# Performance work log

Measured on AMD Instinct MI355X. Metric: run time of the kernel, lower is better.

## Reference

```python
import jax, jax.numpy as jnp
import numpy as np

D_MODEL = 1024
D_INTERNAL = 64
SEQ = 2048
BATCH = 4


def setup_inputs() -> dict:
    key = jax.random.key(0)
    ks = jax.random.split(key, 9)
    s = 1.0 / np.sqrt(D_MODEL)
    return {
        "query": jax.random.normal(ks[0], (SEQ, BATCH, D_MODEL), jnp.float32),
        "key": jax.random.normal(ks[1], (SEQ, BATCH, D_MODEL), jnp.float32),
        "value": jax.random.normal(ks[2], (SEQ, BATCH, D_MODEL), jnp.float32),
        "Wq": jax.random.normal(ks[3], (D_MODEL, D_INTERNAL), jnp.float32) * s,
        "bq": jnp.zeros((D_INTERNAL,), jnp.float32),
        "Wk": jax.random.normal(ks[4], (D_MODEL, D_INTERNAL), jnp.float32) * s,
        "bk": jnp.zeros((D_INTERNAL,), jnp.float32),
        "Wv": jax.random.normal(ks[5], (D_MODEL, D_MODEL), jnp.float32) * s,
        "bv": jnp.zeros((D_MODEL,), jnp.float32),
    }


def reference(query, key, value, Wq, bq, Wk, bk, Wv, bv):
    # inputs: (S, B, D); project then move batch first -> (B, S, *)
    q = (query @ Wq + bq).transpose(1, 0, 2)          # (B, S, d_int)
    k = (key @ Wk + bk).transpose(1, 0, 2)            # (B, S, d_int)
    v = (value @ Wv + bv).transpose(1, 0, 2)          # (B, S, D)
    scores = jnp.einsum("bqd,bkd->bqk", q, k) / jnp.sqrt(jnp.float32(D_INTERNAL))
    probs = jax.nn.softmax(scores, axis=-1)           # row softmax over keys
    # extra renormalization over the QUERY axis (dim=1), as in the source
    probs = probs / (1e-9 + probs.sum(axis=1, keepdims=True))
    aten = jnp.einsum("bqk,bkd->bqd", probs, v).transpose(1, 0, 2)  # (S, B, D)
    return aten, probs
```

## Files before the change

### kernel.cpp

```cpp
#include <hip/hip_runtime.h>
#include <math.h>

#define SEQ 2048
#define BATCH 4
#define DM 1024
#define DI 64

typedef __attribute__((ext_vector_type(8))) short bf16x8;
typedef __attribute__((ext_vector_type(4))) float f32x4;

__device__ __forceinline__ unsigned short f2bf(float f) {
  unsigned u = __float_as_uint(f);
  unsigned r = (u + 0x7fff + ((u >> 16) & 1)) >> 16;
  return (unsigned short)r;
}

__device__ __forceinline__ float bf2f(unsigned short u) {
  return __uint_as_float((unsigned)u << 16);
}

__device__ __forceinline__ void gload_lds16(const void* g, void* l) {
  __builtin_amdgcn_global_load_lds(
      (const __attribute__((address_space(1))) unsigned int*)g,
      (__attribute__((address_space(3))) unsigned int*)l, 16, 0, 0);
}


__global__ __launch_bounds__(256) void trans_kernel(
    const float* __restrict__ Wq, const float* __restrict__ Wk,
    const float* __restrict__ Wv,
    unsigned short* __restrict__ WqkT, unsigned short* __restrict__ WvT) {
  __shared__ unsigned short t[64][65];
  int lx = threadIdx.x & 63, ly = threadIdx.x >> 6;
  if (blockIdx.y < 16) {
    int bx = blockIdx.x * 64, by = blockIdx.y * 64;
#pragma unroll
    for (int i = 0; i < 64; i += 4)
      t[ly + i][lx] = f2bf(Wv[(size_t)(bx + ly + i) * DM + by + lx]);
    __syncthreads();
#pragma unroll
    for (int i = 0; i < 64; i += 4)
      WvT[(size_t)(by + ly + i) * DM + bx + lx] = t[lx][ly + i];
  } else {
    int which = blockIdx.y - 16;
    const float* W = which ? Wk : Wq;
    unsigned short* WT = WqkT + (size_t)which * DI * DM;
    int bx = blockIdx.x * 64;
#pragma unroll
    for (int i = 0; i < 64; i += 4)
      t[ly + i][lx] = f2bf(W[(size_t)(bx + ly + i) * DI + lx]);
    __syncthreads();
#pragma unroll
    for (int i = 0; i < 64; i += 4)
      WT[(size_t)(ly + i) * DM + bx + lx] = t[lx][ly + i];
  }
}

__global__ __launch_bounds__(256) void qkproj_mfma(
    const float* __restrict__ query, const float* __restrict__ key,
    const unsigned short* __restrict__ WqkT,
    const float* __restrict__ bq, const float* __restrict__ bk,
    unsigned short* __restrict__ qbf, unsigned short* __restrict__ kbf) {
  __shared__ __align__(16) unsigned short As[32 * 32];
  __shared__ __align__(16) unsigned short Bs[64 * 32];
  int which = blockIdx.y;
  const float* A = (which ? key : query) + (size_t)blockIdx.x * 32 * DM;
  const unsigned short* Bt = WqkT + (size_t)which * DI * DM;
  const float* bias = which ? bk : bq;
  unsigned short* outp = which ? kbf : qbf;

  const int tid = threadIdx.x;
  const int lane = tid & 63, wave = tid >> 6;
  const int lrow = lane & 15, quad = lane >> 4;
  const int wr = (wave >> 1) * 16;
  const int wc = (wave & 1) * 32;
  const int sw = (quad ^ ((lrow >> 1) & 3)) * 8;
  f32x4 acc[2] = {};

  const int am = tid >> 3, asub = tid & 7;
  const int akc = asub * 4;
  const int asl = am * 32 + (((asub >> 1) ^ ((am >> 1) & 3)) * 8) + (asub & 1) * 4;
  const int bn = tid >> 2;
  const int bkc = (((tid & 3) ^ ((bn >> 1) & 3)) * 8);

  for (int k0 = 0; k0 < DM; k0 += 32) {
    __syncthreads();
    gload_lds16(Bt + (size_t)bn * DM + k0 + bkc, Bs + wave * 512);
    float4 a = *(const float4*)(A + (size_t)am * DM + k0 + akc);
    ushort4 h;
    h.x = f2bf(a.x); h.y = f2bf(a.y); h.z = f2bf(a.z); h.w = f2bf(a.w);
    *(ushort4*)&As[asl] = h;
    __syncthreads();
    bf16x8 af = *(const bf16x8*)&As[(wr + lrow) * 32 + sw];
    bf16x8 b0 = *(const bf16x8*)&Bs[(wc + lrow) * 32 + sw];
    bf16x8 b1 = *(const bf16x8*)&Bs[(wc + 16 + lrow) * 32 + sw];
    acc[0] = __builtin_amdgcn_mfma_f32_16x16x32_bf16(af, b0, acc[0], 0, 0, 0);
    acc[1] = __builtin_amdgcn_mfma_f32_16x16x32_bf16(af, b1, acc[1], 0, 0, 0);
  }
  int sbase = blockIdx.x * 8 + (wr >> 2) + quad;
#pragma unroll
  for (int ni = 0; ni < 2; ++ni) {
    int n = wc + ni * 16 + lrow;
    float bb = bias[n];
#pragma unroll
    for (int reg = 0; reg < 4; ++reg)
      outp[((size_t)reg * SEQ + sbase) * DI + n] = f2bf(acc[ni][reg] + bb);
  }
}

__global__ __launch_bounds__(256) void vcast_kernel(
    const float* __restrict__ value, unsigned short* __restrict__ vbf) {
  size_t i = ((size_t)blockIdx.x * 256 + threadIdx.x) * 8;
  float4 a = *(const float4*)(value + i);
  float4 b = *(const float4*)(value + i + 4);
  bf16x8 h;
  h[0] = (short)f2bf(a.x); h[1] = (short)f2bf(a.y);
  h[2] = (short)f2bf(a.z); h[3] = (short)f2bf(a.w);
  h[4] = (short)f2bf(b.x); h[5] = (short)f2bf(b.y);
  h[6] = (short)f2bf(b.z); h[7] = (short)f2bf(b.w);
  *(bf16x8*)(vbf + i) = h;
}

__device__ __forceinline__ void mfma_core_bb_12864(
    const unsigned short* __restrict__ At, int lda,
    const unsigned short* __restrict__ Bt, int ldb,
    int K, f32x4 (&acc)[4][2],
    unsigned short* As, unsigned short* Bs) {
  const int tid  = threadIdx.x;
  const int lane = tid & 63;
  const int wave = tid >> 6;
  const int wr   = (wave >> 1) * 64;
  const int wc   = (wave & 1) * 32;
  const int lrow = lane & 15;
  const int quad = lane >> 4;
  const int sw   = (quad ^ ((lrow >> 1) & 3)) * 8;
  const int bn   = tid >> 2;
  const int bkc  = ((tid & 3) ^ ((bn >> 1) & 3)) * 8;

  for (int k0 = 0; k0 < K; k0 += 32) {
    __syncthreads();
#pragma unroll
    for (int it = 0; it < 2; ++it) {
      int c = it * 256 + tid;
      int m = c >> 2, kc = ((c & 3) ^ ((m >> 1) & 3)) * 8;
      gload_lds16(At + (size_t)m * lda + k0 + kc,
                  As + (size_t)(it * 256 + wave * 64) * 8);
    }
    gload_lds16(Bt + (size_t)bn * ldb + k0 + bkc, Bs + wave * 512);
    __syncthreads();
    bf16x8 af[4], bfr[2];
#pragma unroll
    for (int mi = 0; mi < 4; ++mi)
      af[mi] = *(const bf16x8*)&As[(wr + mi * 16 + lrow) * 32 + sw];
#pragma unroll
    for (int ni = 0; ni < 2; ++ni)
      bfr[ni] = *(const bf16x8*)&Bs[(wc + ni * 16 + lrow) * 32 + sw];
#pragma unroll
    for (int mi = 0; mi < 4; ++mi)
#pragma unroll
      for (int ni = 0; ni < 2; ++ni)
        acc[mi][ni] = __builtin_amdgcn_mfma_f32_16x16x32_bf16(
            af[mi], bfr[ni], acc[mi][ni], 0, 0, 0);
  }
}

__global__ __launch_bounds__(256) void vproj_mfma(
    const unsigned short* __restrict__ vbf, const unsigned short* __restrict__ WvT,
    const float* __restrict__ bv, unsigned short* __restrict__ vT) {
  __shared__ __align__(16) unsigned short As[128 * 32];
  __shared__ __align__(16) unsigned short Bs[64 * 32];
  __shared__ __align__(16) unsigned short ep[64 * 4 * 32];
  f32x4 acc[4][2] = {};
  int m0 = blockIdx.x * 128, n0 = blockIdx.y * 64;
  mfma_core_bb_12864(vbf + (size_t)m0 * DM, DM, WvT + (size_t)n0 * DM, DM, DM,
                     acc, As, Bs);
  const int tid = threadIdx.x;
  const int lane = tid & 63, wave = tid >> 6;
  const int wr = (wave >> 1) * 64, wc = (wave & 1) * 32;
  const int lrow = lane & 15, quad = lane >> 4;
#pragma unroll
  for (int mi = 0; mi < 4; ++mi) {
    int ss = (wr >> 2) + mi * 4 + quad;
#pragma unroll
    for (int ni = 0; ni < 2; ++ni) {
      int nn = wc + ni * 16 + lrow;
      float bias = bv[n0 + nn];
      int swz = (nn & 3) << 3;
#pragma unroll
      for (int reg = 0; reg < 4; ++reg)
        ep[nn * 128 + reg * 32 + (ss ^ swz)] = f2bf(acc[mi][ni][reg] + bias);
    }
  }
  __syncthreads();
  int s0 = m0 >> 2;
#pragma unroll
  for (int t8 = 0; t8 < 4; ++t8) {
    int c = t8 * 256 + tid;
    int ss8 = (c & 3) * 8, b = (c >> 2) & 3, nn = c >> 4;
    uint4 vv = *(const uint4*)&ep[nn * 128 + b * 32 + (ss8 ^ ((nn & 3) << 3))];
    *(uint4*)&vT[((size_t)(b * DM + n0 + nn)) * SEQ + s0 + ss8] = vv;
  }
}

__global__ __launch_bounds__(256) void scores_rowpanel(
    const unsigned short* __restrict__ qbf, const unsigned short* __restrict__ kbf,
    unsigned short* __restrict__ ebf, float* __restrict__ invrs) {
  __shared__ __align__(16) unsigned short Qs[16 * 64];
  __shared__ __align__(16) unsigned short Ks[128 * 64];
  __shared__ float red[4][16];
  int bid = blockIdx.x;
  int x = bid & 7, j = bid >> 3;
  int b = x >> 1;
  int q0 = (j * 2 + (x & 1)) * 16;

  const int tid = threadIdx.x;
  const int lane = tid & 63, wave = tid >> 6;
  const int lrow = lane & 15, quad = lane >> 4;
  const int wc = wave * 32;
  const int sw = (quad ^ ((lrow >> 1) & 3)) * 8;
  const unsigned short* Q = qbf + ((size_t)b * SEQ + q0) * DI;
  const unsigned short* Kp = kbf + (size_t)b * SEQ * DI;
  unsigned short* C = ebf + (size_t)b * SEQ * SEQ;

  if (tid < 128) {
    int m = tid >> 3, kk = (tid >> 2) & 1, jj = tid & 3;
    gload_lds16(Q + (size_t)m * DI + kk * 32 + ((jj ^ ((m >> 1) & 3)) * 8),
                Qs + (size_t)(tid & ~63) * 8);
  }

  float rsum[4] = {0.f, 0.f, 0.f, 0.f};
  for (int kt = 0; kt < 16; ++kt) {
    int k0 = kt * 128;
    __syncthreads();
#pragma unroll
    for (int it = 0; it < 4; ++it) {
      int c = it * 256 + tid;
      int n = c >> 3, kk = (c >> 2) & 1, jj = c & 3;
      gload_lds16(Kp + (size_t)(k0 + n) * DI + kk * 32 + ((jj ^ ((n >> 1) & 3)) * 8),
                  Ks + (size_t)(it * 256 + wave * 64) * 8);
    }
    __syncthreads();
    bf16x8 af[2], bfr[2][2];
#pragma unroll
    for (int kk = 0; kk < 2; ++kk) {
      af[kk] = *(const bf16x8*)&Qs[lrow * 64 + kk * 32 + sw];
#pragma unroll
      for (int ni = 0; ni < 2; ++ni)
        bfr[ni][kk] = *(const bf16x8*)&Ks[(wc + ni * 16 + lrow) * 64 + kk * 32 + sw];
    }
    f32x4 acc[2] = {};
#pragma unroll
    for (int ni = 0; ni < 2; ++ni) {
      acc[ni] = __builtin_amdgcn_mfma_f32_16x16x32_bf16(af[0], bfr[ni][0], acc[ni], 0, 0, 0);
      acc[ni] = __builtin_amdgcn_mfma_f32_16x16x32_bf16(af[1], bfr[ni][1], acc[ni], 0, 0, 0);
    }
#pragma unroll
    for (int ni = 0; ni < 2; ++ni) {
      int n = k0 + wc + ni * 16 + lrow;
#pragma unroll
      for (int reg = 0; reg < 4; ++reg) {
        float e = __expf(acc[ni][reg] * 0.125f);
        C[(size_t)(q0 + quad * 4 + reg) * SEQ + n] = f2bf(e);
        rsum[reg] += e;
      }
    }
  }
#pragma unroll
  for (int reg = 0; reg < 4; ++reg) {
    rsum[reg] += __shfl_xor(rsum[reg], 1);
    rsum[reg] += __shfl_xor(rsum[reg], 2);
    rsum[reg] += __shfl_xor(rsum[reg], 4);
    rsum[reg] += __shfl_xor(rsum[reg], 8);
  }
  if (lrow == 0) {
#pragma unroll
    for (int reg = 0; reg < 4; ++reg) red[wave][quad * 4 + reg] = rsum[reg];
  }
  __syncthreads();
  if (tid < 16) {
    float t = red[0][tid] + red[1][tid] + red[2][tid] + red[3][tid];
    invrs[(size_t)b * SEQ + q0 + tid] = 1.0f / t;
  }
}

__global__ void zero_kernel(float* __restrict__ p, int n) {
  int i = blockIdx.x * blockDim.x + threadIdx.x;
  if (i < n) p[i] = 0.f;
}

__global__ void recip_kernel(const float* __restrict__ in,
                             float* __restrict__ outp, float eps, int n) {
  int i = blockIdx.x * blockDim.x + threadIdx.x;
  if (i < n) outp[i] = 1.0f / (eps + in[i]);
}

__global__ __launch_bounds__(256) void colsum_kernel(
    const unsigned short* __restrict__ ebf, const float* __restrict__ invrs,
    float* __restrict__ colsum) {
  int b = blockIdx.z;
  int k = blockIdx.x * 256 + threadIdx.x;
  int q0 = blockIdx.y * 128;
  const unsigned short* p = ebf + (size_t)b * SEQ * SEQ + (size_t)q0 * SEQ + k;
  const float* ir = invrs + (size_t)b * SEQ + q0;
  float sum = 0.f;
#pragma unroll 4
  for (int i = 0; i < 128; ++i) sum += bf2f(p[(size_t)i * SEQ]) * ir[i];
  atomicAdd(&colsum[b * SEQ + k], sum);
}

__global__ __launch_bounds__(256) void vscale_kernel(
    unsigned short* __restrict__ vT, const float* __restrict__ invcol) {
  size_t i = ((size_t)blockIdx.x * 256 + threadIdx.x) * 8;
  int s = (int)(i & (SEQ - 1));
  int b = (int)(i >> 21);
  bf16x8 v = *(const bf16x8*)(vT + i);
  const float* ic = invcol + (size_t)b * SEQ + s;
  float4 c0 = *(const float4*)(ic);
  float4 c1 = *(const float4*)(ic + 4);
  bf16x8 r;
  r[0] = (short)f2bf(bf2f((unsigned short)v[0]) * c0.x);
  r[1] = (short)f2bf(bf2f((unsigned short)v[1]) * c0.y);
  r[2] = (short)f2bf(bf2f((unsigned short)v[2]) * c0.z);
  r[3] = (short)f2bf(bf2f((unsigned short)v[3]) * c0.w);
  r[4] = (short)f2bf(bf2f((unsigned short)v[4]) * c1.x);
  r[5] = (short)f2bf(bf2f((unsigned short)v[5]) * c1.y);
  r[6] = (short)f2bf(bf2f((unsigned short)v[6]) * c1.z);
  r[7] = (short)f2bf(bf2f((unsigned short)v[7]) * c1.w);
  *(bf16x8*)(vT + i) = r;
}

__global__ __launch_bounds__(256) void probsout_kernel(
    const unsigned short* __restrict__ ebf, const float* __restrict__ invrs,
    const float* __restrict__ invcol, float* __restrict__ probs) {
  size_t f = ((size_t)blockIdx.x * 256 + threadIdx.x) * 4;
  int b = (int)(f >> 22);
  int q = (int)((f >> 11) & 2047);
  int k = (int)(f & 2047);
  ushort4 h = *(const ushort4*)(ebf + f);
  float ir = invrs[b * SEQ + q];
  float4 c = *(const float4*)(invcol + b * SEQ + k);
  float4 p;
  p.x = bf2f(h.x) * ir * c.x;
  p.y = bf2f(h.y) * ir * c.y;
  p.z = bf2f(h.z) * ir * c.z;
  p.w = bf2f(h.w) * ir * c.w;
  *(float4*)(probs + f) = p;
}

__global__ __launch_bounds__(256) void aten_mfma(
    const unsigned short* __restrict__ ebf, const unsigned short* __restrict__ vT,
    const float* __restrict__ invrs, float* __restrict__ out) {
  __shared__ __align__(16) unsigned short As[128 * 64];
  __shared__ __align__(16) unsigned short Bs[128 * 64];
  __shared__ float irs[128];
  int bid = blockIdx.x;
  int wg = (bid & 7) * 64 + (bid >> 3);
  int mb = wg & 15, nb = (wg >> 4) & 7, b = wg >> 7;
  int m0 = mb * 128, n0 = nb * 128;
  if (threadIdx.x < 128)
    irs[threadIdx.x] = invrs[(size_t)b * SEQ + m0 + threadIdx.x];
  const unsigned short* At = ebf + ((size_t)b * SEQ + m0) * SEQ;
  const unsigned short* Bt = vT + ((size_t)b * DM + n0) * SEQ;

  const int tid = threadIdx.x;
  const int lane = tid & 63, wave = tid >> 6;
  const int wr = (wave >> 1) * 64, wc = (wave & 1) * 64;
  const int lrow = lane & 15, quad = lane >> 4;
  const int sw = (quad ^ ((lrow >> 1) & 3)) * 8;

  f32x4 acc[4][4] = {};
  for (int k0 = 0; k0 < SEQ; k0 += 64) {
    __syncthreads();
#pragma unroll
    for (int it = 0; it < 4; ++it) {
      int c = it * 256 + tid;
      int m = c >> 3, kk = (c >> 2) & 1, jj = c & 3;
      gload_lds16(At + (size_t)m * SEQ + k0 + kk * 32 + ((jj ^ ((m >> 1) & 3)) * 8),
                  As + (size_t)(it * 256 + wave * 64) * 8);
    }
#pragma unroll
    for (int it = 0; it < 4; ++it) {
      int c = it * 256 + tid;
      int n = c >> 3, kk = (c >> 2) & 1, jj = c & 3;
      gload_lds16(Bt + (size_t)n * SEQ + k0 + kk * 32 + ((jj ^ ((n >> 1) & 3)) * 8),
                  Bs + (size_t)(it * 256 + wave * 64) * 8);
    }
    __syncthreads();
    bf16x8 bfr[4][2];
#pragma unroll
    for (int ni = 0; ni < 4; ++ni)
#pragma unroll
      for (int kk = 0; kk < 2; ++kk)
        bfr[ni][kk] = *(const bf16x8*)&Bs[(wc + ni * 16 + lrow) * 64 + kk * 32 + sw];
#pragma unroll
    for (int mi = 0; mi < 4; ++mi) {
      bf16x8 a0 = *(const bf16x8*)&As[(wr + mi * 16 + lrow) * 64 + sw];
      bf16x8 a1 = *(const bf16x8*)&As[(wr + mi * 16 + lrow) * 64 + 32 + sw];
#pragma unroll
      for (int ni = 0; ni < 4; ++ni) {
        acc[mi][ni] = __builtin_amdgcn_mfma_f32_16x16x32_bf16(a0, bfr[ni][0], acc[mi][ni], 0, 0, 0);
        acc[mi][ni] = __builtin_amdgcn_mfma_f32_16x16x32_bf16(a1, bfr[ni][1], acc[mi][ni], 0, 0, 0);
      }
    }
  }
#pragma unroll
  for (int mi = 0; mi < 4; ++mi) {
    int rb = wr + mi * 16 + quad * 4;
    int qr = m0 + rb;
#pragma unroll
    for (int ni = 0; ni < 4; ++ni) {
      int n = n0 + wc + ni * 16 + lrow;
#pragma unroll
      for (int reg = 0; reg < 4; ++reg)
        out[(size_t)(qr + reg) * (BATCH * DM) + b * DM + n] =
            acc[mi][ni][reg] * irs[rb + reg];
    }
  }
}

extern "C" void kernel_launch(void* const* d_in, const int* in_sizes, int n_in,
                              void* d_out, int out_size, void* d_ws, size_t ws_size,
                              hipStream_t stream) {
  const float* query = (const float*)d_in[0];
  const float* key   = (const float*)d_in[1];
  const float* value = (const float*)d_in[2];
  const float* Wq    = (const float*)d_in[3];
  const float* bq    = (const float*)d_in[4];
  const float* Wk    = (const float*)d_in[5];
  const float* bk    = (const float*)d_in[6];
  const float* Wv    = (const float*)d_in[7];
  const float* bv    = (const float*)d_in[8];

  float* out   = (float*)d_out;
  float* probs = out + (size_t)SEQ * BATCH * DM;

  unsigned short* WvT  = (unsigned short*)d_ws;
  unsigned short* WqkT = WvT  + (size_t)DM * DM;
  unsigned short* qbf  = WqkT + (size_t)2 * DI * DM;
  unsigned short* kbf  = qbf  + (size_t)BATCH * SEQ * DI;
  unsigned short* vT   = kbf  + (size_t)BATCH * SEQ * DI;
  unsigned short* ebf  = vT   + (size_t)BATCH * DM * SEQ;
  unsigned short* vbf  = ebf;
  float* colsum = (float*)(ebf + (size_t)BATCH * SEQ * SEQ);
  float* invrs  = colsum + (size_t)BATCH * SEQ;
  float* invcol = invrs  + (size_t)BATCH * SEQ;

  trans_kernel<<<dim3(16, 18), 256, 0, stream>>>(Wq, Wk, Wv, WqkT, WvT);
  qkproj_mfma<<<dim3(SEQ * BATCH / 32, 2), 256, 0, stream>>>(
      query, key, WqkT, bq, bk, qbf, kbf);
  vcast_kernel<<<(SEQ * BATCH * DM / 8) / 256, 256, 0, stream>>>(value, vbf);
  vproj_mfma<<<dim3(SEQ * BATCH / 128, DM / 64), 256, 0, stream>>>(vbf, WvT, bv, vT);
  scores_rowpanel<<<dim3(512), 256, 0, stream>>>(qbf, kbf, ebf, invrs);
  zero_kernel<<<(BATCH * SEQ + 255) / 256, 256, 0, stream>>>(colsum, BATCH * SEQ);
  colsum_kernel<<<dim3(SEQ / 256, SEQ / 128, BATCH), 256, 0, stream>>>(
      ebf, invrs, colsum);
  recip_kernel<<<(BATCH * SEQ + 255) / 256, 256, 0, stream>>>(
      colsum, invcol, 1e-9f, BATCH * SEQ);
  vscale_kernel<<<(BATCH * DM * SEQ / 8) / 256, 256, 0, stream>>>(vT, invcol);
  aten_mfma<<<dim3(512), 256, 0, stream>>>(ebf, vT, invrs, out);
  probsout_kernel<<<(BATCH * SEQ * SEQ / 4) / 256, 256, 0, stream>>>(
      ebf, invrs, invcol, probs);
}
```

Measured before the change: 327.3 us.

## Fuse column-sum into scores kernel and column scaling into V projection

The column-sum pass over the exp-score matrix is folded into the scores kernel, where each block re-reads its freshly written 16-row panel and atomically adds scaled column partials. The V-projection epilogue now multiplies by the inverse column sums, so the separate vscale pass over vT is removed. The colsum zeroing moves into the weight-transpose kernel. vbf gets its own workspace region so the V projection can run after the scores. This cuts three launches and two full passes over large buffers. In exchange there are more atomics (8 per thread per block), a re-read of the panel inside the scores kernel, and a larger workspace.

Result: slower. 334.2 us (+2.1%).

```diff
diff --git a/kernel.cpp b/kernel.cpp
--- a/kernel.cpp
+++ b/kernel.cpp
@@ -29,7 +29,8 @@
 __global__ __launch_bounds__(256) void trans_kernel(
     const float* __restrict__ Wq, const float* __restrict__ Wk,
     const float* __restrict__ Wv,
-    unsigned short* __restrict__ WqkT, unsigned short* __restrict__ WvT) {
+    unsigned short* __restrict__ WqkT, unsigned short* __restrict__ WvT,
+    float* __restrict__ colsum) {
   __shared__ unsigned short t[64][65];
   int lx = threadIdx.x & 63, ly = threadIdx.x >> 6;
   if (blockIdx.y < 16) {
@@ -41,7 +42,7 @@
 #pragma unroll
     for (int i = 0; i < 64; i += 4)
       WvT[(size_t)(by + ly + i) * DM + bx + lx] = t[lx][ly + i];
-  } else {
+  } else if (blockIdx.y < 18) {
     int which = blockIdx.y - 16;
     const float* W = which ? Wk : Wq;
     unsigned short* WT = WqkT + (size_t)which * DI * DM;
@@ -53,6 +54,10 @@
 #pragma unroll
     for (int i = 0; i < 64; i += 4)
       WT[(size_t)(ly + i) * DM + bx + lx] = t[lx][ly + i];
+  } else {
+    int idx = blockIdx.x * 256 + threadIdx.x;
+    colsum[idx] = 0.f;
+    colsum[idx + 4096] = 0.f;
   }
 }
 
@@ -166,12 +171,17 @@
 
 __global__ __launch_bounds__(256) void vproj_mfma(
     const unsigned short* __restrict__ vbf, const unsigned short* __restrict__ WvT,
-    const float* __restrict__ bv, unsigned short* __restrict__ vT) {
+    const float* __restrict__ bv, const float* __restrict__ invcol,
+    unsigned short* __restrict__ vT) {
   __shared__ __align__(16) unsigned short As[128 * 32];
   __shared__ __align__(16) unsigned short Bs[64 * 32];
   __shared__ __align__(16) unsigned short ep[64 * 4 * 32];
+  __shared__ float icl[128];
   f32x4 acc[4][2] = {};
   int m0 = blockIdx.x * 128, n0 = blockIdx.y * 64;
+  int s0 = m0 >> 2;
+  if (threadIdx.x < 128)
+    icl[threadIdx.x] = invcol[(size_t)(threadIdx.x >> 5) * SEQ + s0 + (threadIdx.x & 31)];
   mfma_core_bb_12864(vbf + (size_t)m0 * DM, DM, WvT + (size_t)n0 * DM, DM, DM,
                      acc, As, Bs);
   const int tid = threadIdx.x;
@@ -188,11 +198,11 @@
       int swz = (nn & 3) << 3;
 #pragma unroll
       for (int reg = 0; reg < 4; ++reg)
-        ep[nn * 128 + reg * 32 + (ss ^ swz)] = f2bf(acc[mi][ni][reg] + bias);
+        ep[nn * 128 + reg * 32 + (ss ^ swz)] =
+            f2bf((acc[mi][ni][reg] + bias) * icl[reg * 32 + ss]);
     }
   }
   __syncthreads();
-  int s0 = m0 >> 2;
 #pragma unroll
   for (int t8 = 0; t8 < 4; ++t8) {
     int c = t8 * 256 + tid;
@@ -204,10 +214,12 @@
 
 __global__ __launch_bounds__(256) void scores_rowpanel(
     const unsigned short* __restrict__ qbf, const unsigned short* __restrict__ kbf,
-    unsigned short* __restrict__ ebf, float* __restrict__ invrs) {
+    unsigned short* __restrict__ ebf, float* __restrict__ invrs,
+    float* __restrict__ colsum) {
   __shared__ __align__(16) unsigned short Qs[16 * 64];
   __shared__ __align__(16) unsigned short Ks[128 * 64];
   __shared__ float red[4][16];
+  __shared__ float irl[16];
   int bid = blockIdx.x;
   int x = bid & 7, j = bid >> 3;
   int b = x >> 1;
@@ -265,6 +277,7 @@
       }
     }
   }
+  __threadfence_block();
 #pragma unroll
   for (int reg = 0; reg < 4; ++reg) {
     rsum[reg] += __shfl_xor(rsum[reg], 1);
@@ -279,54 +292,33 @@
   __syncthreads();
   if (tid < 16) {
     float t = red[0][tid] + red[1][tid] + red[2][tid] + red[3][tid];
-    invrs[(size_t)b * SEQ + q0 + tid] = 1.0f / t;
-  }
-}
-
-__global__ void zero_kernel(float* __restrict__ p, int n) {
-  int i = blockIdx.x * blockDim.x + threadIdx.x;
-  if (i < n) p[i] = 0.f;
+    float inv = 1.0f / t;
+    invrs[(size_t)b * SEQ + q0 + tid] = inv;
+    irl[tid] = inv;
+  }
+  __syncthreads();
+  int k8 = tid * 8;
+  float cs[8] = {0.f, 0.f, 0.f, 0.f, 0.f, 0.f, 0.f, 0.f};
+#pragma unroll 4
+  for (int i = 0; i < 16; ++i) {
+    const unsigned short* row = C + (size_t)(q0 + i) * SEQ + k8;
+    ushort4 h0 = *(const ushort4*)(row);
+    ushort4 h1 = *(const ushort4*)(row + 4);
+    float ir = irl[i];
+    cs[0] += bf2f(h0.x) * ir; cs[1] += bf2f(h0.y) * ir;
+    cs[2] += bf2f(h0.z) * ir; cs[3] += bf2f(h0.w) * ir;
+    cs[4] += bf2f(h1.x) * ir; cs[5] += bf2f(h1.y) * ir;
+    cs[6] += bf2f(h1.z) * ir; cs[7] += bf2f(h1.w) * ir;
+  }
+#pragma unroll
+  for (int jj = 0; jj < 8; ++jj)
+    atomicAdd(&colsum[b * SEQ + k8 + jj], cs[jj]);
 }
 
 __global__ void recip_kernel(const float* __restrict__ in,
                              float* __restrict__ outp, float eps, int n) {
   int i = blockIdx.x * blockDim.x + threadIdx.x;
   if (i < n) outp[i] = 1.0f / (eps + in[i]);
-}
-
-__global__ __launch_bounds__(256) void colsum_kernel(
-    const unsigned short* __restrict__ ebf, const float* __restrict__ invrs,
-    float* __restrict__ colsum) {
-  int b = blockIdx.z;
-  int k = blockIdx.x * 256 + threadIdx.x;
-  int q0 = blockIdx.y * 128;
-  const unsigned short* p = ebf + (size_t)b * SEQ * SEQ + (size_t)q0 * SEQ + k;
-  const float* ir = invrs + (size_t)b * SEQ + q0;
-  float sum = 0.f;
-#pragma unroll 4
-  for (int i = 0; i < 128; ++i) sum += bf2f(p[(size_t)i * SEQ]) * ir[i];
-  atomicAdd(&colsum[b * SEQ + k], sum);
-}
-
-__global__ __launch_bounds__(256) void vscale_kernel(
-    unsigned short* __restrict__ vT, const float* __restrict__ invcol) {
-  size_t i = ((size_t)blockIdx.x * 256 + threadIdx.x) * 8;
-  int s = (int)(i & (SEQ - 1));
-  int b = (int)(i >> 21);
-  bf16x8 v = *(const bf16x8*)(vT + i);
-  const float* ic = invcol + (size_t)b * SEQ + s;
-  float4 c0 = *(const float4*)(ic);
-  float4 c1 = *(const float4*)(ic + 4);
-  bf16x8 r;
-  r[0] = (short)f2bf(bf2f((unsigned short)v[0]) * c0.x);
-  r[1] = (short)f2bf(bf2f((unsigned short)v[1]) * c0.y);
-  r[2] = (short)f2bf(bf2f((unsigned short)v[2]) * c0.z);
-  r[3] = (short)f2bf(bf2f((unsigned short)v[3]) * c0.w);
-  r[4] = (short)f2bf(bf2f((unsigned short)v[4]) * c1.x);
-  r[5] = (short)f2bf(bf2f((unsigned short)v[5]) * c1.y);
-  r[6] = (short)f2bf(bf2f((unsigned short)v[6]) * c1.z);
-  r[7] = (short)f2bf(bf2f((unsigned short)v[7]) * c1.w);
-  *(bf16x8*)(vT + i) = r;
 }
 
 __global__ __launch_bounds__(256) void probsout_kernel(
@@ -440,23 +432,20 @@
   unsigned short* kbf  = qbf  + (size_t)BATCH * SEQ * DI;
   unsigned short* vT   = kbf  + (size_t)BATCH * SEQ * DI;
   unsigned short* ebf  = vT   + (size_t)BATCH * DM * SEQ;
-  unsigned short* vbf  = ebf;
-  float* colsum = (float*)(ebf + (size_t)BATCH * SEQ * SEQ);
+  unsigned short* vbf  = ebf  + (size_t)BATCH * SEQ * SEQ;
+  float* colsum = (float*)(vbf + (size_t)BATCH * SEQ * DM);
   float* invrs  = colsum + (size_t)BATCH * SEQ;
   float* invcol = invrs  + (size_t)BATCH * SEQ;
 
-  trans_kernel<<<dim3(16, 18), 256, 0, stream>>>(Wq, Wk, Wv, WqkT, WvT);
+  trans_kernel<<<dim3(16, 19), 256, 0, stream>>>(Wq, Wk, Wv, WqkT, WvT, colsum);
   qkproj_mfma<<<dim3(SEQ * BATCH / 32, 2), 256, 0, stream>>>(
       query, key, WqkT, bq, bk, qbf, kbf);
   vcast_kernel<<<(SEQ * BATCH * DM / 8) / 256, 256, 0, stream>>>(value, vbf);
-  vproj_mfma<<<dim3(SEQ * BATCH / 128, DM / 64), 256, 0, stream>>>(vbf, WvT, bv, vT);
-  scores_rowpanel<<<dim3(512), 256, 0, stream>>>(qbf, kbf, ebf, invrs);
-  zero_kernel<<<(BATCH * SEQ + 255) / 256, 256, 0, stream>>>(colsum, BATCH * SEQ);
-  colsum_kernel<<<dim3(SEQ / 256, SEQ / 128, BATCH), 256, 0, stream>>>(
-      ebf, invrs, colsum);
+  scores_rowpanel<<<dim3(512), 256, 0, stream>>>(qbf, kbf, ebf, invrs, colsum);
   recip_kernel<<<(BATCH * SEQ + 255) / 256, 256, 0, stream>>>(
       colsum, invcol, 1e-9f, BATCH * SEQ);
-  vscale_kernel<<<(BATCH * DM * SEQ / 8) / 256, 256, 0, stream>>>(vT, invcol);
+  vproj_mfma<<<dim3(SEQ * BATCH / 128, DM / 64), 256, 0, stream>>>(
+      vbf, WvT, bv, invcol, vT);
   aten_mfma<<<dim3(512), 256, 0, stream>>>(ebf, vT, invrs, out);
   probsout_kernel<<<(BATCH * SEQ * SEQ / 4) / 256, 256, 0, stream>>>(
       ebf, invrs, invcol, probs);
```
